# Optimization experiments

Hardware: AMD Instinct MI355X
Metric: run time of the kernel (lower is better)

The kernel has to match this reference:

```python
import jax, jax.numpy as jnp
import numpy as np

B, T, C = 2, 1024, 256
DH = 8          # deformable head num
HD = 64         # head_dim
HN = C // HD    # head_num = 4


def grid_sample_bilinear(img, grid):
    """torch.nn.functional.grid_sample (bilinear, align_corners=True) for a
    single-channel image. img: (B,H,W); grid: (B,Ho,Wo,2) with grid[...,0]=x
    (width coord), grid[...,1]=y (height coord), both in [-1,1]."""
    B_, H, W = img.shape
    gx = (grid[..., 0] + 1.0) * 0.5 * (W - 1)
    gy = (grid[..., 1] + 1.0) * 0.5 * (H - 1)
    x0 = jnp.floor(gx)
    y0 = jnp.floor(gy)
    wx = gx - x0
    wy = gy - y0
    flat_img = img.reshape(B_, -1)

    def gather(iy, ix):
        iy = jnp.clip(iy.astype(jnp.int32), 0, H - 1)
        ix = jnp.clip(ix.astype(jnp.int32), 0, W - 1)
        flat = (iy * W + ix).reshape(B_, -1)
        return jnp.take_along_axis(flat_img, flat, axis=1).reshape(iy.shape)

    out = (gather(y0, x0) * (1 - wy) * (1 - wx)
           + gather(y0, x0 + 1) * (1 - wy) * wx
           + gather(y0 + 1, x0) * wy * (1 - wx)
           + gather(y0 + 1, x0 + 1) * wy * wx)
    return out  # (B, Ho, Wo)


def setup_inputs() -> dict:
    key = jax.random.key(0)
    ks = jax.random.split(key, 8)
    s = 1.0 / np.sqrt(C)
    return {
        "x": jax.random.normal(ks[0], (B, T, C), jnp.float32),
        "W_off1": jax.random.normal(ks[1], (C, C), jnp.float32) * s,
        "b_off1": jnp.zeros((C,), jnp.float32),
        "W_off2": jax.random.normal(ks[2], (C, DH * C * 2), jnp.float32) * s,
        "b_off2": jnp.zeros((DH * C * 2,), jnp.float32),
        "Wq": jax.random.normal(ks[3], (C, C), jnp.float32) * s,
        "bq": jnp.zeros((C,), jnp.float32),
        "Wk": jax.random.normal(ks[4], (C, C), jnp.float32) * s,
        "bk": jnp.zeros((C,), jnp.float32),
        "Wv": jax.random.normal(ks[5], (C, C), jnp.float32) * s,
        "bv": jnp.zeros((C,), jnp.float32),
        "Wo": jax.random.normal(ks[6], (DH * C, C), jnp.float32) / np.sqrt(DH * C),
        "bo": jnp.zeros((C,), jnp.float32),
    }


def reference(x, W_off1, b_off1, W_off2, b_off2, Wq, bq, Wk, bk, Wv, bv, Wo, bo):
    B_, T_, C_ = x.shape
    # offset network: per-token MLP -> DH heads of (C,2) grid coords in [-1,1]
    h = jax.nn.gelu(x @ W_off1 + b_off1)
    off = jnp.tanh((h @ W_off2 + b_off2).reshape(B_, T_, DH, C_, 2))
    off = off.transpose(0, 2, 1, 3, 4).reshape(B_, DH * T_, C_, 2)
    # deformable token resampling: x tiled DH times along token axis acts as
    # a 1-channel image of size (DH*T, C); grid_sample(bilinear, align_corners)
    img = jnp.tile(x, (1, DH, 1))                       # B x (DH*T) x C
    xs = grid_sample_bilinear(img, off)                 # B x (DH*T) x C
    xs = xs.reshape(B_ * DH, T_, C_)
    # multi-head attention over resampled tokens
    q = (xs @ Wq + bq).reshape(B_ * DH, T_, HN, HD)
    k = (xs @ Wk + bk).reshape(B_ * DH, T_, HN, HD)
    v = (xs @ Wv + bv).reshape(B_ * DH, T_, HN, HD)
    scores = jnp.einsum('bnhd,bkhd->bhnk', q, k) / np.float32(np.sqrt(HD))
    A = jax.nn.softmax(scores, axis=-1)
    out = jnp.einsum('bhnk,bkhd->bnhd', A, v).reshape(B_ * DH, T_, HN * HD)
    # gather deformable heads back and project
    out = out.reshape(B_, DH, T_, HN * HD).transpose(0, 2, 1, 3).reshape(B_, T_, DH * HN * HD)
    return out @ Wo + bo
```

## Files before the change

### kernel.cpp

```cpp
#include <hip/hip_runtime.h>
#include <hip/hip_bf16.h>

typedef __attribute__((ext_vector_type(8))) _Float16 half8;
typedef __attribute__((ext_vector_type(4))) float f32x4;
typedef __attribute__((ext_vector_type(16))) float f32x16;
typedef __attribute__((ext_vector_type(2))) unsigned uint2v;
typedef __attribute__((ext_vector_type(4))) unsigned uint4v;

#define MFMAH(a, b, c) __builtin_amdgcn_mfma_f32_16x16x32_f16((a), (b), (c), 0, 0, 0)
#define MFMA32(a, b, c) __builtin_amdgcn_mfma_f32_32x32x16_f16((a), (b), (c), 0, 0, 0)

__device__ __forceinline__ short f2h(float v) { _Float16 h = (_Float16)v; return __builtin_bit_cast(short, h); }
__device__ __forceinline__ f32x4 fzero() { f32x4 z = {0.f, 0.f, 0.f, 0.f}; return z; }
__device__ __forceinline__ float u2f(unsigned u) { return __builtin_bit_cast(float, u); }
__device__ __forceinline__ unsigned f2u(float f) { return __builtin_bit_cast(unsigned, f); }

__device__ __forceinline__ void gl16(const void* g, void* l) {
    __builtin_amdgcn_global_load_lds((const __attribute__((address_space(1))) unsigned*)g,
                                     (__attribute__((address_space(3))) unsigned*)l, 16, 0, 0);
}

__device__ __forceinline__ float gelu_tanh(float v) {
    float u = 0.7978845608028654f * (v + 0.044715f * v * v * v);
    return 0.5f * v * (1.f + tanhf(u));
}


__global__ __launch_bounds__(256) void split_w2_k(const float* __restrict__ w, short* __restrict__ dst) {
    __shared__ float t[64][65];
    const int tid = threadIdx.x;
    const int bk = blockIdx.x >> 6, bn = blockIdx.x & 63;
    const int k0 = bk * 64, n0 = bn * 64;
#pragma unroll
    for (int p = 0; p < 16; ++p) {
        int idx = p * 256 + tid, r = idx >> 6, c = idx & 63;
        t[r][c] = w[(long)(k0 + r) * 4096 + n0 + c];
    }
    __syncthreads();
#pragma unroll
    for (int p = 0; p < 16; ++p) {
        int idx = p * 256 + tid, nr = idx >> 6, kc = idx & 63;
        float v = t[kc][nr];
        _Float16 w1 = (_Float16)v;
        _Float16 w2 = (_Float16)(v - (float)w1);
        long base = (long)(n0 + nr) * 768 + k0 + kc;
        dst[base]       = __builtin_bit_cast(short, w1);
        dst[base + 256] = __builtin_bit_cast(short, w1);
        dst[base + 512] = __builtin_bit_cast(short, w2);
    }
}

__global__ void qkv_prep_k(const float* __restrict__ Wq, const float* __restrict__ Wk,
                           const float* __restrict__ Wv, short* __restrict__ dst) {
    int i = blockIdx.x * 256 + threadIdx.x;
    int n = i >> 8, k = i & 255;
    const float* s = (n < 256) ? Wq : (n < 512) ? Wk : Wv;
    dst[i] = f2h(s[k * 256 + (n & 255)]);
}

__global__ void wo_prep_k(const float* __restrict__ Wo, short* __restrict__ dst) {
    int i = blockIdx.x * 256 + threadIdx.x;
    int n = i >> 11, k = i & 2047;
    dst[i] = f2h(Wo[k * 256 + n]);
}


__global__ __launch_bounds__(256) void gemm1_k(const float* __restrict__ x, const float* __restrict__ W,
                                               const float* __restrict__ bias, short* __restrict__ hs) {
    __shared__ float As[64][17];
    __shared__ float Bs[16][68];
    const int tid = threadIdx.x;
    const int bm = blockIdx.x >> 2, bn = blockIdx.x & 3;
    const int m0 = bm * 64, n0 = bn * 64;
    const int ty = tid >> 4, tx = tid & 15;
    float acc[4][4] = {};
    const int ar = tid >> 2, ak = (tid & 3) << 2;
    const int bk = tid >> 4, bc = (tid & 15) << 2;

    for (int k0 = 0; k0 < 256; k0 += 16) {
        __syncthreads();
        float4 av = *(const float4*)(x + (m0 + ar) * 256 + k0 + ak);
        As[ar][ak + 0] = av.x; As[ar][ak + 1] = av.y; As[ar][ak + 2] = av.z; As[ar][ak + 3] = av.w;
        *(float4*)&Bs[bk][bc] = *(const float4*)(W + (k0 + bk) * 256 + n0 + bc);
        __syncthreads();
#pragma unroll
        for (int kk = 0; kk < 16; ++kk) {
            float a_[4], b_[4];
#pragma unroll
            for (int i = 0; i < 4; ++i) a_[i] = As[ty * 4 + i][kk];
            *(float4*)b_ = *(const float4*)&Bs[kk][tx * 4];
#pragma unroll
            for (int i = 0; i < 4; ++i)
#pragma unroll
                for (int j = 0; j < 4; ++j) acc[i][j] += a_[i] * b_[j];
        }
    }
#pragma unroll
    for (int i = 0; i < 4; ++i) {
        int row = m0 + ty * 4 + i;
#pragma unroll
        for (int j = 0; j < 4; ++j) {
            int col = n0 + tx * 4 + j;
            float v = gelu_tanh(acc[i][j] + bias[col]);
            _Float16 h1 = (_Float16)v;
            _Float16 h2 = (_Float16)(v - (float)h1);
            hs[row * 768 + col]       = __builtin_bit_cast(short, h1);
            hs[row * 768 + 256 + col] = __builtin_bit_cast(short, h2);
            hs[row * 768 + 512 + col] = __builtin_bit_cast(short, h1);
        }
    }
}


template <int EPI>
__global__ __launch_bounds__(256, 2) void gemm128(
    const short* __restrict__ A, const short* __restrict__ BT,
    const float* __restrict__ b0, const float* __restrict__ b1, const float* __restrict__ b2,
    void* __restrict__ out0, void* __restrict__ out1, void* __restrict__ out2,
    int M, int N, int K, int lda, int ldb, const float* __restrict__ xsrc)
{
    __shared__ short lds[16384];
    short* As0 = lds;
    short* As1 = lds + 4096;
    short* Bs0 = lds + 8192;
    short* Bs1 = lds + 12288;

    const int tid = threadIdx.x;
    const int lane = tid & 63, w = tid >> 6;
    const int rl = lane & 15, g = lane >> 4;
    const int wr = w >> 1, wc = w & 1;
    const int bid = blockIdx.x;
    int bm, bn;
    if (EPI == 1) {
        bm = bid >> 5;
        bn = (bid & 7) * 4 + ((bid >> 3) & 3);
    } else if (EPI == 2) {
        int s = bid >> 3;
        bm = (bid & 7) * 16 + s / 6;
        bn = s - (s / 6) * 6;
    } else {
        const int nb = N >> 7;
        bm = bid / nb;
        bn = bid % nb;
    }
    const int m0 = bm << 7, n0 = bn << 7;

    if (EPI == 3) { A += blockIdx.y << 8; BT += blockIdx.y << 8; }

    f32x4 acc[4][4];
#pragma unroll
    for (int m = 0; m < 4; ++m)
#pragma unroll
        for (int n = 0; n < 4; ++n) acc[m][n] = fzero();

    const short* ap = A + (long)(m0 + w * 32 + (lane >> 2)) * lda + ((lane & 3) << 3);
    const short* bp = BT + (long)(n0 + w * 32 + (lane >> 2)) * ldb + ((lane & 3) << 3);
    const int woff = w * 1024;

#define STAGE(dA, dB, kk) do { \
        gl16(ap + (kk), (dA) + woff); \
        gl16(ap + (kk) + 16 * lda, (dA) + woff + 512); \
        gl16(bp + (kk), (dB) + woff); \
        gl16(bp + (kk) + 16 * ldb, (dB) + woff + 512); } while (0)

    const int nt_ = K >> 5;
    STAGE(As0, Bs0, 0);
    __syncthreads();
    for (int t = 0; t < nt_; ++t) {
        const short* cA = (t & 1) ? As1 : As0;
        const short* cB = (t & 1) ? Bs1 : Bs0;
        short* nA = (t & 1) ? As0 : As1;
        short* nB = (t & 1) ? Bs0 : Bs1;
        if (t + 1 < nt_) STAGE(nA, nB, (t + 1) << 5);
        half8 af[4], bf[4];
#pragma unroll
        for (int m = 0; m < 4; ++m) af[m] = *(const half8*)&cA[(wr * 64 + m * 16 + rl) * 32 + g * 8];
#pragma unroll
        for (int n = 0; n < 4; ++n) bf[n] = *(const half8*)&cB[(wc * 64 + n * 16 + rl) * 32 + g * 8];
#pragma unroll
        for (int m = 0; m < 4; ++m)
#pragma unroll
            for (int n = 0; n < 4; ++n) acc[m][n] = MFMAH(af[m], bf[n], acc[m][n]);
        __syncthreads();
    }
#undef STAGE

    if (EPI == 1) {
        const int d = n0 >> 9, c0 = (n0 >> 1) & 255;
#pragma unroll
        for (int m = 0; m < 4; ++m)
#pragma unroll
            for (int nt = 0; nt < 4; ++nt) {
                const int col = n0 + wc * 64 + nt * 16 + rl;
                float o4[4], po4[4];
                const float bb = b0[col];
#pragma unroll
                for (int j = 0; j < 4; ++j) o4[j] = tanhf(acc[m][nt][j] + bb);
#pragma unroll
                for (int j = 0; j < 4; ++j) po4[j] = __shfl_xor(o4[j], 1);
                const int jlo = (rl & 1) ? 2 : 0;
                const int cl = (wc * 64 + nt * 16 + rl) >> 1;
#pragma unroll
                for (int u = 0; u < 2; ++u) {
                    const int j = jlo + u;
                    float gx = (rl & 1) ? po4[j] : o4[j];
                    float gy = (rl & 1) ? o4[j] : po4[j];
                    gx = (gx + 1.f) * 127.5f;
                    gy = (gy + 1.f) * 4095.5f;
                    float x0f = floorf(gx), y0f = floorf(gy);
                    float wx = gx - x0f, wy = gy - y0f;
                    int ix0 = (int)x0f, iy0 = (int)y0f;
                    int ix1 = min(ix0 + 1, 255), iy1 = min(iy0 + 1, 8191);
                    ix0 = max(min(ix0, 255), 0);
                    iy0 = max(min(iy0, 8191), 0);
                    ix1 = max(ix1, 0);
                    iy1 = max(iy1, 0);
                    const int rowl = wr * 64 + m * 16 + g * 4 + j;
                    const int b = (m0 + rowl) >> 10;
                    const float* xb = xsrc + b * 262144;
                    int r0 = (iy0 & 1023) << 8, r1 = (iy1 & 1023) << 8;
                    float v00 = xb[r0 + ix0], v01 = xb[r0 + ix1];
                    float v10 = xb[r1 + ix0], v11 = xb[r1 + ix1];
                    float r = v00 * (1.f - wy) * (1.f - wx) + v01 * (1.f - wy) * wx
                            + v10 * wy * (1.f - wx) + v11 * wy * wx;
                    lds[rowl * 72 + cl] = f2h(r);
                }
            }
        __syncthreads();
        const int b = m0 >> 10, t0 = m0 & 1023;
        short* xo = (short*)out0 + ((long)(b * 8 + d) * 1024 + t0) * 256 + c0;
#pragma unroll
        for (int p = 0; p < 4; ++p) {
            int idx = p * 256 + tid, rowl = idx >> 3, ch = idx & 7;
            *(half8*)(xo + rowl * 256 + ch * 8) = *(const half8*)&lds[rowl * 72 + ch * 8];
        }
    } else if (EPI == 2) {
#pragma unroll
        for (int m = 0; m < 4; ++m)
#pragma unroll
            for (int nt = 0; nt < 4; ++nt) {
                const int cl = wc * 64 + nt * 16 + rl;
                const int col = n0 + cl;
#pragma unroll
                for (int j = 0; j < 4; ++j) {
                    const int tl = wr * 64 + m * 16 + g * 4 + j;
                    float v;
                    int slot;
                    if (bn < 2) {
                        v = (acc[m][nt][j] + b0[col]) * 0.18033688011112042f;
                        slot = tl * 128 + cl;
                    } else if (bn < 4) {
                        v = acc[m][nt][j] + b1[(bn - 2) * 128 + cl];
                        int hl = cl >> 6, dd = cl & 63;
                        int c = dd >> 4, hi2 = (dd >> 3) & 1, e = dd & 7;
                        int kkl = tl >> 5, l31t = tl & 31;
                        slot = (hl * 4 + kkl) * 2048 + (c * 64 + hi2 * 32 + l31t) * 8 + e;
                    } else {
                        v = acc[m][nt][j] + b2[(bn - 4) * 128 + cl];
                        int hl = cl >> 6, d = cl & 63;
                        int kkl = tl >> 5, chi = (tl >> 4) & 1, hi2 = (tl >> 3) & 1, e = tl & 7;
                        int c = chi * 2 + (d >> 5);
                        slot = (hl * 4 + kkl) * 2048 + (c * 64 + hi2 * 32 + (d & 31)) * 8 + e;
                    }
                    lds[slot] = f2h(v);
                }
            }
        __syncthreads();
        const int bh = m0 >> 10;
        if (bn < 2) {
            short* qo = (short*)out0 + (long)m0 * 256 + n0;
#pragma unroll
            for (int p = 0; p < 8; ++p) {
                int idx = p * 256 + tid, rowl = idx >> 4, ch = idx & 15;
                *(half8*)(qo + rowl * 256 + ch * 8) = *(const half8*)&lds[rowl * 128 + ch * 8];
            }
        } else {
            short* dst = (bn < 4) ? (short*)out1 : (short*)out2;
            const int hb = (bn < 4) ? (bn - 2) * 2 : (bn - 4) * 2;
            const int kk0 = (m0 & 1023) >> 5;
#pragma unroll
            for (int p = 0; p < 8; ++p) {
                int idx = p * 256 + tid, til = idx >> 8, wit = idx & 255;
                int hl = til >> 2, kkl = til & 3;
                long base = (((long)(bh * 4 + hb + hl) * 32) + kk0 + kkl) * 2048;
                *(half8*)(dst + base + wit * 8) = *(const half8*)&lds[til * 2048 + wit * 8];
            }
        }
    } else {
        float* op = (float*)out0 + (long)blockIdx.y * M * N;
#pragma unroll
        for (int m = 0; m < 4; ++m)
#pragma unroll
            for (int nt = 0; nt < 4; ++nt) {
                const int col = n0 + wc * 64 + nt * 16 + rl;
#pragma unroll
                for (int j = 0; j < 4; ++j) {
                    const long grow = m0 + wr * 64 + m * 16 + g * 4 + j;
                    op[grow * N + col] = acc[m][nt][j];
                }
            }
    }
}

__global__ void reduce_out_k(const float* __restrict__ p, const float* __restrict__ bo,
                             float* __restrict__ out) {
    int i = blockIdx.x * 256 + threadIdx.x;
    float s = bo[i & 255];
#pragma unroll
    for (int ks = 0; ks < 8; ++ks) s += p[ks * 524288 + i];
    out[i] = s;
}


__global__ __launch_bounds__(256) void attn_k(const short* __restrict__ q, const short* __restrict__ kc,
                                              const short* __restrict__ vc, short* __restrict__ oc) {
    __shared__ short kv[8192];
    const int tid = threadIdx.x;
    const int lane = tid & 63, w = tid >> 6;
    const int l31 = lane & 31, hi = lane >> 5;
    const int bhh = blockIdx.x & 63;
    const int bh = bhh >> 2, h = bhh & 3;
    const int q0 = (blockIdx.x >> 6) * 128 + w * 32;

    const short* qb = q + (long)bh * 262144 + h * 64;
    const short* kt = kc + (long)bhh * 65536;
    const short* vt = vc + (long)bhh * 65536;

    half8 qf[4];
#pragma unroll
    for (int c = 0; c < 4; ++c)
        qf[c] = *(const half8*)(qb + (long)(q0 + l31) * 256 + c * 16 + hi * 8);

    float m_ = -1e30f, l_ = 0.f;
    f32x16 O0, O1;
#pragma unroll
    for (int r = 0; r < 16; ++r) { O0[r] = 0.f; O1[r] = 0.f; }

    const int sw = w * 512 + lane * 8;

#define KVSTAGE(kk, b) do { \
        gl16(kt + (kk) * 2048 + sw, &kv[(b) * 4096 + w * 512]); \
        gl16(vt + (kk) * 2048 + sw, &kv[(b) * 4096 + 2048 + w * 512]); } while (0)

    KVSTAGE(0, 0);
    __syncthreads();
    for (int kk = 0; kk < 32; ++kk) {
        const int b = kk & 1;
        if (kk + 1 < 32) KVSTAGE(kk + 1, b ^ 1);
        half8 KD[4], VD[4];
#pragma unroll
        for (int c = 0; c < 4; ++c) {
            KD[c] = *(const half8*)&kv[b * 4096 + c * 512 + lane * 8];
            VD[c] = *(const half8*)&kv[b * 4096 + 2048 + c * 512 + lane * 8];
        }
        f32x16 S;
#pragma unroll
        for (int r = 0; r < 16; ++r) S[r] = 0.f;
#pragma unroll
        for (int c = 0; c < 4; ++c) S = MFMA32(KD[c], qf[c], S);
        float t8[8];
#pragma unroll
        for (int r = 0; r < 8; ++r) t8[r] = fmaxf(S[2 * r], S[2 * r + 1]);
        float mx = fmaxf(fmaxf(fmaxf(t8[0], t8[1]), fmaxf(t8[2], t8[3])),
                         fmaxf(fmaxf(t8[4], t8[5]), fmaxf(t8[6], t8[7])));
        uint2v sp = __builtin_amdgcn_permlane32_swap(f2u(mx), f2u(mx), false, false);
        mx = fmaxf(u2f(sp[0]), u2f(sp[1]));
        if (__any(mx > m_ + 8.f)) {
            float mn = fmaxf(m_, mx);
            float sc = exp2f(m_ - mn);
            m_ = mn;
            l_ *= sc;
#pragma unroll
            for (int r = 0; r < 16; ++r) { O0[r] *= sc; O1[r] *= sc; }
        }
        float p[16];
#pragma unroll
        for (int r = 0; r < 16; ++r) p[r] = exp2f(S[r] - m_);
        float s8[8];
#pragma unroll
        for (int r = 0; r < 8; ++r) s8[r] = p[2 * r] + p[2 * r + 1];
        float rs = (((s8[0] + s8[1]) + (s8[2] + s8[3])) + ((s8[4] + s8[5]) + (s8[6] + s8[7])));
        uint2v sq = __builtin_amdgcn_permlane32_swap(f2u(rs), f2u(rs), false, false);
        rs = u2f(sq[0]) + u2f(sq[1]);
        l_ += rs;
        half8 PA[2];
#pragma unroll
        for (int c = 0; c < 2; ++c) {
            const int o = c * 8;
            unsigned a0 = f2u(__builtin_bit_cast(float, __builtin_amdgcn_cvt_pkrtz(p[o + 0], p[o + 1])));
            unsigned b0v = f2u(__builtin_bit_cast(float, __builtin_amdgcn_cvt_pkrtz(p[o + 4], p[o + 5])));
            unsigned a1 = f2u(__builtin_bit_cast(float, __builtin_amdgcn_cvt_pkrtz(p[o + 2], p[o + 3])));
            unsigned b1v = f2u(__builtin_bit_cast(float, __builtin_amdgcn_cvt_pkrtz(p[o + 6], p[o + 7])));
            uint2v r0 = __builtin_amdgcn_permlane32_swap(a0, b0v, false, false);
            uint2v r1 = __builtin_amdgcn_permlane32_swap(a1, b1v, false, false);
            uint4v wpk = {r0[0], r1[0], r0[1], r1[1]};
            PA[c] = __builtin_bit_cast(half8, wpk);
        }
        O0 = MFMA32(VD[0], PA[0], O0);
        O1 = MFMA32(VD[1], PA[0], O1);
        O0 = MFMA32(VD[2], PA[1], O0);
        O1 = MFMA32(VD[3], PA[1], O1);
        __syncthreads();
    }
#undef KVSTAGE

    const float inv = 1.f / l_;
    const int b = bh >> 3, d = bh & 7;
    const int t = q0 + l31;
    short* ob = oc + ((long)(b * 1024 + t) * 8 + d) * 256 + h * 64;
#pragma unroll
    for (int rr = 0; rr < 8; ++rr) {
        int dvb = (rr & 1) * 2 + 8 * (rr >> 1) + 4 * hi;
        unsigned u0 = (unsigned short)f2h(O0[2 * rr] * inv) | ((unsigned)(unsigned short)f2h(O0[2 * rr + 1] * inv) << 16);
        unsigned u1 = (unsigned short)f2h(O1[2 * rr] * inv) | ((unsigned)(unsigned short)f2h(O1[2 * rr + 1] * inv) << 16);
        *(unsigned*)(ob + dvb) = u0;
        *(unsigned*)(ob + 32 + dvb) = u1;
    }
}


extern "C" void kernel_launch(void* const* d_in, const int* in_sizes, int n_in,
                              void* d_out, int out_size, void* d_ws, size_t ws_size,
                              hipStream_t stream) {
    const float* x     = (const float*)d_in[0];
    const float* Woff1 = (const float*)d_in[1];
    const float* boff1 = (const float*)d_in[2];
    const float* Woff2 = (const float*)d_in[3];
    const float* boff2 = (const float*)d_in[4];
    const float* Wq    = (const float*)d_in[5];
    const float* bq    = (const float*)d_in[6];
    const float* Wk    = (const float*)d_in[7];
    const float* bk    = (const float*)d_in[8];
    const float* Wv    = (const float*)d_in[9];
    const float* bv    = (const float*)d_in[10];
    const float* Wo    = (const float*)d_in[11];
    const float* bo    = (const float*)d_in[12];

    char* ws = (char*)d_ws;
    short* hsplit = (short*)(ws + 0);
    short* B2T    = (short*)(ws + 3145728);
    short* cat    = (short*)(ws + 0);
    short* Wtqkv  = (short*)(ws + 9437184);
    short* WtoT   = (short*)(ws + 9830400);
    short* xs     = (short*)(ws + 10878976);
    short* qbuf   = (short*)(ws + 19267584);
    short* kcoal  = (short*)(ws + 27656192);
    short* vcoal  = (short*)(ws + 36044800);
    float* parts  = (float*)(ws + 44433408);

    split_w2_k<<<256, 256, 0, stream>>>(Woff2, B2T);
    qkv_prep_k<<<768, 256, 0, stream>>>(Wq, Wk, Wv, Wtqkv);
    wo_prep_k<<<2048, 256, 0, stream>>>(Wo, WtoT);

    gemm1_k<<<128, 256, 0, stream>>>(x, Woff1, boff1, hsplit);

    gemm128<1><<<(2048 / 128) * (4096 / 128), 256, 0, stream>>>(
        hsplit, B2T, boff2, nullptr, nullptr, xs, nullptr, nullptr, 2048, 4096, 768, 768, 768, x);

    gemm128<2><<<(16384 / 128) * (768 / 128), 256, 0, stream>>>(
        xs, Wtqkv, bq, bk, bv, qbuf, kcoal, vcoal, 16384, 768, 256, 256, 256, nullptr);

    attn_k<<<512, 256, 0, stream>>>(qbuf, kcoal, vcoal, cat);

    gemm128<3><<<dim3((2048 / 128) * (256 / 128), 8), 256, 0, stream>>>(
        cat, WtoT, nullptr, nullptr, nullptr, parts, nullptr, nullptr, 2048, 256, 256, 2048, 2048, nullptr);
    reduce_out_k<<<2048, 256, 0, stream>>>(parts, bo, (float*)d_out);
}
```

Baseline: 165.0 us.

## Replace GEMM syncthreads with vmcnt waits, fast tanh, paired bilinear gathers

The GEMM main loop now issues the next stage's async LDS loads and then waits only for the older ones with an explicit s_waitcnt vmcnt before a raw s_barrier. This replaces the full __syncthreads drains and lets the prefetch overlap with the MFMAs. tanhf in GELU and in the offset epilogue becomes an exp-based fast tanh. The bilinear sampling also fetches each horizontal pixel pair with one 8-byte load instead of two scalar loads. These changes cut memory-wait and transcendental cost, but they depend on exact vmcnt accounting and trade some precision for speed.

```diff
diff --git a/kernel.cpp b/kernel.cpp
--- a/kernel.cpp
+++ b/kernel.cpp
@@ -6,6 +6,7 @@
 typedef __attribute__((ext_vector_type(16))) float f32x16;
 typedef __attribute__((ext_vector_type(2))) unsigned uint2v;
 typedef __attribute__((ext_vector_type(4))) unsigned uint4v;
+typedef __attribute__((ext_vector_type(2), aligned(4))) float f32x2a;
 
 #define MFMAH(a, b, c) __builtin_amdgcn_mfma_f32_16x16x32_f16((a), (b), (c), 0, 0, 0)
 #define MFMA32(a, b, c) __builtin_amdgcn_mfma_f32_32x32x16_f16((a), (b), (c), 0, 0, 0)
@@ -20,9 +21,14 @@
                                      (__attribute__((address_space(3))) unsigned*)l, 16, 0, 0);
 }
 
+__device__ __forceinline__ float fast_tanh(float z) {
+    float E = __expf(2.f * z);
+    return 1.f - 2.f / (E + 1.f);
+}
+
 __device__ __forceinline__ float gelu_tanh(float v) {
     float u = 0.7978845608028654f * (v + 0.044715f * v * v * v);
-    return 0.5f * v * (1.f + tanhf(u));
+    return 0.5f * v * (1.f + fast_tanh(u));
 }
 
 
@@ -165,13 +171,18 @@
 
     const int nt_ = K >> 5;
     STAGE(As0, Bs0, 0);
-    __syncthreads();
     for (int t = 0; t < nt_; ++t) {
         const short* cA = (t & 1) ? As1 : As0;
         const short* cB = (t & 1) ? Bs1 : Bs0;
         short* nA = (t & 1) ? As0 : As1;
         short* nB = (t & 1) ? Bs0 : Bs1;
-        if (t + 1 < nt_) STAGE(nA, nB, (t + 1) << 5);
+        if (t + 1 < nt_) {
+            STAGE(nA, nB, (t + 1) << 5);
+            asm volatile("s_waitcnt vmcnt(4)" ::: "memory");
+        } else {
+            asm volatile("s_waitcnt vmcnt(0)" ::: "memory");
+        }
+        __builtin_amdgcn_s_barrier();
         half8 af[4], bf[4];
 #pragma unroll
         for (int m = 0; m < 4; ++m) af[m] = *(const half8*)&cA[(wr * 64 + m * 16 + rl) * 32 + g * 8];
@@ -181,7 +192,7 @@
         for (int m = 0; m < 4; ++m)
 #pragma unroll
             for (int n = 0; n < 4; ++n) acc[m][n] = MFMAH(af[m], bf[n], acc[m][n]);
-        __syncthreads();
+        __builtin_amdgcn_s_barrier();
     }
 #undef STAGE
 
@@ -195,7 +206,7 @@
                 float o4[4], po4[4];
                 const float bb = b0[col];
 #pragma unroll
-                for (int j = 0; j < 4; ++j) o4[j] = tanhf(acc[m][nt][j] + bb);
+                for (int j = 0; j < 4; ++j) o4[j] = fast_tanh(acc[m][nt][j] + bb);
 #pragma unroll
                 for (int j = 0; j < 4; ++j) po4[j] = __shfl_xor(o4[j], 1);
                 const int jlo = (rl & 1) ? 2 : 0;
@@ -210,17 +221,20 @@
                     float x0f = floorf(gx), y0f = floorf(gy);
                     float wx = gx - x0f, wy = gy - y0f;
                     int ix0 = (int)x0f, iy0 = (int)y0f;
-                    int ix1 = min(ix0 + 1, 255), iy1 = min(iy0 + 1, 8191);
-                    ix0 = max(min(ix0, 255), 0);
+                    int iy1 = min(iy0 + 1, 8191);
                     iy0 = max(min(iy0, 8191), 0);
-                    ix1 = max(ix1, 0);
                     iy1 = max(iy1, 0);
+                    int ixc = max(min(ix0, 254), 0);
                     const int rowl = wr * 64 + m * 16 + g * 4 + j;
                     const int b = (m0 + rowl) >> 10;
                     const float* xb = xsrc + b * 262144;
                     int r0 = (iy0 & 1023) << 8, r1 = (iy1 & 1023) << 8;
-                    float v00 = xb[r0 + ix0], v01 = xb[r0 + ix1];
-                    float v10 = xb[r1 + ix0], v11 = xb[r1 + ix1];
+                    f32x2a fx0 = *(const f32x2a*)(xb + r0 + ixc);
+                    f32x2a fx1 = *(const f32x2a*)(xb + r1 + ixc);
+                    float v00 = (ix0 >= 255) ? fx0[1] : fx0[0];
+                    float v01 = (ix0 < 0)    ? fx0[0] : fx0[1];
+                    float v10 = (ix0 >= 255) ? fx1[1] : fx1[0];
+                    float v11 = (ix0 < 0)    ? fx1[0] : fx1[1];
                     float r = v00 * (1.f - wy) * (1.f - wx) + v01 * (1.f - wy) * wx
                             + v10 * wy * (1.f - wx) + v11 * wy * wx;
                     lds[rowl * 72 + cl] = f2h(r);
```

After: 155.9 us. -5.5%, faster.
